# Kernel optimization log

Measured on AMD Instinct MI355X. Metric: run time of the kernel, lower is better.

The kernel has to match this reference:

```python
import jax, jax.numpy as jnp
import numpy as np

N = 50000      # nodes (src == dst, num_layers=1)
F_IN = 256     # feats_dim
HID = 128      # hidden_dim
H = 8          # num_heads
D = HID // H   # per-head dim
E = 800000     # edges per metapath
M = 3          # metapaths
OUT = 8        # out_dim
NEG_SLOPE = 0.2


def setup_inputs() -> dict:
    key = jax.random.key(0)
    ks = jax.random.split(key, 14)
    s = 0.05
    return {
        "features": jax.random.normal(ks[0], (N, F_IN), jnp.float32),
        "W_fc": jax.random.normal(ks[1], (F_IN, HID), jnp.float32) * s,
        "b_fc": jnp.zeros((HID,), jnp.float32),
        "W_src": jax.random.normal(ks[2], (M, HID, HID), jnp.float32) * s,
        "W_dst": jax.random.normal(ks[3], (M, HID, HID), jnp.float32) * s,
        "attn_l": jax.random.normal(ks[4], (M, H, D), jnp.float32) * s,
        "attn_r": jax.random.normal(ks[5], (M, H, D), jnp.float32) * s,
        "W_sem1": jax.random.normal(ks[6], (HID, HID), jnp.float32) * s,
        "b_sem1": jnp.zeros((HID,), jnp.float32),
        "w_sem2": jax.random.normal(ks[7], (HID,), jnp.float32) * s,
        "W_out": jax.random.normal(ks[8], (HID, OUT), jnp.float32) * s,
        "b_out": jnp.zeros((OUT,), jnp.float32),
        "src_idx": jax.random.randint(ks[9], (M, E), 0, N, jnp.int32),
        "dst_idx": jax.random.randint(ks[10], (M, E), 0, N, jnp.int32),
    }


def _gat_conv(h, Wsrc, Wdst, al, ar, src, dst):
    # h: (N, HID); per-metapath GATConv with tuple in_feats (separate src/dst fc)
    fs = (h @ Wsrc).reshape(N, H, D)   # src projected features
    fd = (h @ Wdst).reshape(N, H, D)   # dst projected features
    el = jnp.sum(fs * al, axis=-1)     # (N, H)
    er = jnp.sum(fd * ar, axis=-1)     # (N, H)
    e = jax.nn.leaky_relu(el[src] + er[dst], NEG_SLOPE)  # (E, H)
    # edge softmax segmented by destination node
    mx = jax.ops.segment_max(e, dst, num_segments=N)     # (N, H)
    ex = jnp.exp(e - mx[dst])
    ssum = jax.ops.segment_sum(ex, dst, num_segments=N)  # (N, H)
    alpha = ex / jnp.maximum(ssum[dst], 1e-9)            # (E, H)
    # weighted message aggregation (gather -> scale -> scatter-add)
    out = jax.ops.segment_sum(fs[src] * alpha[:, :, None], dst, num_segments=N)
    return out.reshape(N, HID)


def reference(features, W_fc, b_fc, W_src, W_dst, attn_l, attn_r,
              W_sem1, b_sem1, w_sem2, W_out, b_out, src_idx, dst_idx):
    h_ = features @ W_fc + b_fc                          # (N, HID)
    outs = []
    for m in range(M):  # small fixed loop over metapaths
        hm = _gat_conv(h_, W_src[m], W_dst[m], attn_l[m], attn_r[m],
                       src_idx[m], dst_idx[m])
        outs.append(jax.nn.elu(hm))
    z = jnp.stack(outs, axis=1)                          # (N, M, HID)
    # semantic attention over metapaths
    w = jnp.tanh(z @ W_sem1 + b_sem1) @ w_sem2           # (N, M)
    beta = jax.nn.softmax(w, axis=1)
    fused = jnp.sum(beta[:, :, None] * z, axis=1)        # (N, HID)
    logits = fused @ W_out + b_out                       # (N, OUT)
    return logits
```

## Files before the change

kernel.cpp:

```cpp
#include <hip/hip_runtime.h>
#include <hip/hip_bf16.h>
#include <stdint.h>

#define N_NODES 50000
#define F_IN 256
#define HID 128
#define NH 8
#define DH 16
#define NE 800000
#define NM 3
#define NOUT 8
#define NEG 0.2f
#define NROWS (N_NODES * NM)
#define LDH 136
#define BSH 8
#define NBUCK 196
#define EPB 8192

#define WFCP_N 65536
#define WSP_N  98304
#define UTP_N  6144
#define W1P_N  16384

typedef __attribute__((ext_vector_type(8))) short bfrag;
typedef __attribute__((ext_vector_type(4))) float f32x4;
union FU { uint4 u; bfrag b; };

#define MFMA(a, b, c) __builtin_amdgcn_mfma_f32_16x16x32_bf16(a, b, c, 0, 0, 0)

__device__ __forceinline__ float bf2f(unsigned short u) {
    union { unsigned int ui; float f; } cv;
    cv.ui = ((unsigned int)u) << 16;
    return cv.f;
}
__device__ __forceinline__ unsigned short f2bf(float x) {
    __hip_bfloat16 b = __float2bfloat16(x);
    return reinterpret_cast<const unsigned short&>(b);
}
__device__ __forceinline__ float bflo(unsigned int u) {
    union { unsigned int x; float f; } c; c.x = u << 16; return c.f;
}
__device__ __forceinline__ float bfhi(unsigned int u) {
    union { unsigned int x; float f; } c; c.x = u & 0xffff0000u; return c.f;
}

__global__ __launch_bounds__(256) void k_bhist(const int* __restrict__ dst0,
                                               int* __restrict__ bcnt) {
    __shared__ int cnt[NBUCK];
    int m = blockIdx.y;
    const int* dst = dst0 + (size_t)m * NE;
    int t = threadIdx.x;
    int e0 = blockIdx.x * EPB;
    int e1 = e0 + EPB; if (e1 > NE) e1 = NE;
    for (int i = t; i < NBUCK; i += 256) cnt[i] = 0;
    __syncthreads();
    for (int i = e0 + t; i < e1; i += 256)
        atomicAdd(&cnt[dst[i] >> BSH], 1);
    __syncthreads();
    for (int i = t; i < NBUCK; i += 256)
        if (cnt[i]) atomicAdd(&bcnt[m * NBUCK + i], cnt[i]);
}

__global__ __launch_bounds__(256) void k_bscan(const int* __restrict__ bcnt,
                                               int* __restrict__ bbase,
                                               int* __restrict__ binCur) {
    __shared__ int sc[256];
    int m = blockIdx.x, t = threadIdx.x;
    int v = (t < NBUCK) ? bcnt[m * NBUCK + t] : 0;
    sc[t] = v;
    __syncthreads();
    #pragma unroll
    for (int o = 1; o < 256; o <<= 1) {
        int add = (t >= o) ? sc[t - o] : 0;
        __syncthreads();
        sc[t] += add;
        __syncthreads();
    }
    if (t < NBUCK) {
        int p = sc[t] - v;
        bbase[m * NBUCK + t] = p;
        binCur[m * NBUCK + t] = p;
    }
}

__global__ __launch_bounds__(256) void k_binA2(const int* __restrict__ src0,
                                               const int* __restrict__ dst0,
                                               int* __restrict__ binCur0,
                                               int2* __restrict__ pairs0) {
    __shared__ int cnt[NBUCK];
    __shared__ int base[NBUCK];
    int m = blockIdx.y;
    const int* src = src0 + (size_t)m * NE;
    const int* dst = dst0 + (size_t)m * NE;
    int* binCur = binCur0 + (size_t)m * NBUCK;
    int2* pairs = pairs0 + (size_t)m * NE;
    int t = threadIdx.x;
    int e0 = blockIdx.x * EPB;
    int e1 = e0 + EPB; if (e1 > NE) e1 = NE;
    for (int i = t; i < NBUCK; i += 256) cnt[i] = 0;
    __syncthreads();
    for (int i = e0 + t; i < e1; i += 256)
        atomicAdd(&cnt[dst[i] >> BSH], 1);
    __syncthreads();
    for (int i = t; i < NBUCK; i += 256) {
        int c = cnt[i];
        base[i] = c ? atomicAdd(&binCur[i], c) : 0;
        cnt[i] = 0;
    }
    __syncthreads();
    for (int i = e0 + t; i < e1; i += 256) {
        int d = dst[i], s = src[i];
        int b = d >> BSH;
        int off = atomicAdd(&cnt[b], 1);
        pairs[base[b] + off] = make_int2(s, d);
    }
}

__global__ __launch_bounds__(256) void k_csr(const int2* __restrict__ pairs0,
                                             const int* __restrict__ bcnt,
                                             const int* __restrict__ bbase,
                                             int* __restrict__ offs0,
                                             int* __restrict__ ssrc0) {
    __shared__ int cnt[256];
    __shared__ int cur[256];
    int b = blockIdx.x, m = blockIdx.y, t = threadIdx.x;
    const int2* pairs = pairs0 + (size_t)m * NE;
    int* offs = offs0 + (size_t)m * (N_NODES + 1);
    int* ssrc = ssrc0 + (size_t)m * NE;
    int pbase = bbase[m * NBUCK + b];
    int pend  = pbase + bcnt[m * NBUCK + b];
    cnt[t] = 0;
    __syncthreads();
    for (int i = pbase + t; i < pend; i += 256)
        atomicAdd(&cnt[pairs[i].y & 255], 1);
    __syncthreads();
    int v = cnt[t];
    __syncthreads();
    #pragma unroll
    for (int o = 1; o < 256; o <<= 1) {
        int add = (t >= o) ? cnt[t - o] : 0;
        __syncthreads();
        cnt[t] += add;
        __syncthreads();
    }
    int ex = cnt[t] - v;
    int dst0 = b << BSH;
    int nd = N_NODES - dst0; if (nd > 256) nd = 256;
    if (t < nd) offs[dst0 + t] = pbase + ex;
    if (b == NBUCK - 1 && t == 0) offs[N_NODES] = NE;
    cur[t] = pbase + ex;
    __syncthreads();
    for (int i = pbase + t; i < pend; i += 256) {
        int2 p = pairs[i];
        int pos = atomicAdd(&cur[p.y & 255], 1);
        ssrc[pos] = p.x;
    }
}

__global__ __launch_bounds__(256) void k_pack(const float* __restrict__ Wfc,
                                              const float* __restrict__ Wsrc,
                                              const float* __restrict__ Wdst,
                                              const float* __restrict__ al,
                                              const float* __restrict__ ar,
                                              const float* __restrict__ Wsem1,
                                              unsigned short* __restrict__ wfcph,
                                              unsigned short* __restrict__ wfcpl,
                                              unsigned short* __restrict__ wsph,
                                              unsigned short* __restrict__ wspl,
                                              unsigned short* __restrict__ utph,
                                              unsigned short* __restrict__ utpl,
                                              unsigned short* __restrict__ w1ph,
                                              unsigned short* __restrict__ w1pl) {
    int g = blockIdx.x * 256 + threadIdx.x;
    if (blockIdx.x < 16) {
        int s = g;
        int lane = s & 63, t = s >> 6;
        int ks = t & 7, ct = t >> 3;
        int n = ct * 16 + (lane & 15);
        int kb = ks * 32 + ((lane >> 4) << 3);
        #pragma unroll
        for (int j = 0; j < 8; j++) {
            float v = Wfc[(size_t)(kb + j) * HID + n];
            unsigned short h = f2bf(v);
            wfcph[(size_t)s * 8 + j] = h;
            wfcpl[(size_t)s * 8 + j] = f2bf(v - bf2f(h));
        }
    } else if (blockIdx.x < 40) {
        int s = g - 16 * 256;
        int lane = s & 63, t = s >> 6;
        int ks = t & 3, ct = (t >> 2) & 7, m = t >> 5;
        int n = ct * 16 + (lane & 15);
        int kb = ks * 32 + ((lane >> 4) << 3);
        #pragma unroll
        for (int j = 0; j < 8; j++) {
            float v = Wsrc[((size_t)m * HID + kb + j) * HID + n];
            unsigned short h = f2bf(v);
            wsph[(size_t)s * 8 + j] = h;
            wspl[(size_t)s * 8 + j] = f2bf(v - bf2f(h));
        }
    } else if (blockIdx.x < 43) {
        int s = g - 40 * 256;
        if (s >= UTP_N / 8) return;
        int lane = s & 63, t = s >> 6;
        int ks = t & 3, m = t >> 2;
        int n = lane & 15;
        int kb = ks * 32 + ((lane >> 4) << 3);
        int hh = n & 7;
        const float* W = (n < 8) ? Wsrc : Wdst;
        const float* a = (n < 8) ? al : ar;
        #pragma unroll
        for (int j = 0; j < 8; j++) {
            int k = kb + j;
            const float* wr = W + ((size_t)m * HID + k) * HID + hh * DH;
            const float* av = a + m * HID + hh * DH;
            float v = 0.f;
            #pragma unroll
            for (int d = 0; d < DH; d++) v += wr[d] * av[d];
            unsigned short h = f2bf(v);
            utph[(size_t)s * 8 + j] = h;
            utpl[(size_t)s * 8 + j] = f2bf(v - bf2f(h));
        }
    } else {
        int s = g - 43 * 256;
        int lane = s & 63, t = s >> 6;
        int ks = t & 3, ct = t >> 2;
        int n = ct * 16 + (lane & 15);
        int kb = ks * 32 + ((lane >> 4) << 3);
        #pragma unroll
        for (int j = 0; j < 8; j++) {
            float v = Wsem1[(size_t)(kb + j) * HID + n];
            unsigned short h = f2bf(v);
            w1ph[(size_t)s * 8 + j] = h;
            w1pl[(size_t)s * 8 + j] = f2bf(v - bf2f(h));
        }
    }
}

__global__ __launch_bounds__(256) void k_fcproj(const float* __restrict__ A,
                                                const float* __restrict__ bias,
                                                const unsigned short* __restrict__ wfcph,
                                                const unsigned short* __restrict__ wfcpl,
                                                const unsigned short* __restrict__ wsph,
                                                const unsigned short* __restrict__ wspl,
                                                const unsigned short* __restrict__ utph,
                                                const unsigned short* __restrict__ utpl,
                                                unsigned short* __restrict__ fs0,
                                                float* __restrict__ el0,
                                                float* __restrict__ er0) {
    __shared__ unsigned short hb[64 * LDH];
    int tid = threadIdx.x;
    int w = tid >> 6, l = tid & 63;
    int rw = w & 1;
    int ch = w >> 1;
    int lr = l & 15;
    int lq = l >> 4;
    int r0 = blockIdx.x * 64;
    int gr[2];
    #pragma unroll
    for (int rt = 0; rt < 2; rt++) {
        int rowA = r0 + rw * 32 + rt * 16 + lr;
        gr[rt] = (rowA < N_NODES) ? rowA : (N_NODES - 1);
    }

    f32x4 acc[2][4];
    #pragma unroll
    for (int rt = 0; rt < 2; rt++)
        #pragma unroll
        for (int c = 0; c < 4; c++) acc[rt][c] = (f32x4){0.f, 0.f, 0.f, 0.f};
    const uint4* bh4 = (const uint4*)wfcph;
    const uint4* bl4 = (const uint4*)wfcpl;
    for (int ks = 0; ks < 8; ks++) {
        bfrag ah[2], al_[2];
        #pragma unroll
        for (int rt = 0; rt < 2; rt++) {
            const float* ap = A + (size_t)gr[rt] * F_IN + ks * 32 + lq * 8;
            float4 v0 = ((const float4*)ap)[0];
            float4 v1 = ((const float4*)ap)[1];
            float av[8] = {v0.x, v0.y, v0.z, v0.w, v1.x, v1.y, v1.z, v1.w};
            #pragma unroll
            for (int j = 0; j < 8; j++) {
                unsigned short h = f2bf(av[j]);
                ah[rt][j] = (short)h;
                al_[rt][j] = (short)f2bf(av[j] - bf2f(h));
            }
        }
        #pragma unroll
        for (int c = 0; c < 4; c++) {
            int ct = ch * 4 + c;
            FU bh, bl;
            bh.u = bh4[(ct * 8 + ks) * 64 + l];
            bl.u = bl4[(ct * 8 + ks) * 64 + l];
            #pragma unroll
            for (int rt = 0; rt < 2; rt++) {
                acc[rt][c] = MFMA(ah[rt], bh.b, acc[rt][c]);
                acc[rt][c] = MFMA(ah[rt], bl.b, acc[rt][c]);
                acc[rt][c] = MFMA(al_[rt], bh.b, acc[rt][c]);
            }
        }
    }
    #pragma unroll
    for (int c = 0; c < 4; c++) {
        int col = (ch * 4 + c) * 16 + lr;
        float bb = bias[col];
        #pragma unroll
        for (int rt = 0; rt < 2; rt++)
            #pragma unroll
            for (int rg = 0; rg < 4; rg++) {
                int rloc = rw * 32 + rt * 16 + lq * 4 + rg;
                hb[rloc * LDH + col] = f2bf(acc[rt][c][rg] + bb);
            }
    }
    __syncthreads();
    const uint4* sh4 = (const uint4*)wsph;
    const uint4* sl4 = (const uint4*)wspl;
    const uint4* uh4 = (const uint4*)utph;
    const uint4* ul4 = (const uint4*)utpl;
    for (int m = 0; m < NM; m++) {
        f32x4 acc2[2][4];
        f32x4 eacc[2];
        #pragma unroll
        for (int rt = 0; rt < 2; rt++) {
            eacc[rt] = (f32x4){0.f, 0.f, 0.f, 0.f};
            #pragma unroll
            for (int c = 0; c < 4; c++) acc2[rt][c] = (f32x4){0.f, 0.f, 0.f, 0.f};
        }
        #pragma unroll
        for (int ks = 0; ks < 4; ks++) {
            FU a[2];
            #pragma unroll
            for (int rt = 0; rt < 2; rt++)
                a[rt].u = *(const uint4*)&hb[(rw * 32 + rt * 16 + lr) * LDH + ks * 32 + lq * 8];
            #pragma unroll
            for (int c = 0; c < 4; c++) {
                int ct = ch * 4 + c;
                FU bh, bl;
                bh.u = sh4[(m * 32 + ct * 4 + ks) * 64 + l];
                bl.u = sl4[(m * 32 + ct * 4 + ks) * 64 + l];
                #pragma unroll
                for (int rt = 0; rt < 2; rt++) {
                    acc2[rt][c] = MFMA(a[rt].b, bh.b, acc2[rt][c]);
                    acc2[rt][c] = MFMA(a[rt].b, bl.b, acc2[rt][c]);
                }
            }
            if (ch == 0) {
                FU uh, ul;
                uh.u = uh4[(m * 4 + ks) * 64 + l];
                ul.u = ul4[(m * 4 + ks) * 64 + l];
                #pragma unroll
                for (int rt = 0; rt < 2; rt++) {
                    eacc[rt] = MFMA(a[rt].b, uh.b, eacc[rt]);
                    eacc[rt] = MFMA(a[rt].b, ul.b, eacc[rt]);
                }
            }
        }
        unsigned short* fsm = fs0 + (size_t)m * N_NODES * HID;
        #pragma unroll
        for (int rt = 0; rt < 2; rt++)
            #pragma unroll
            for (int c = 0; c < 4; c++) {
                #pragma unroll
                for (int rg = 0; rg < 4; rg++) {
                    int row = r0 + rw * 32 + rt * 16 + lq * 4 + rg;
                    if (row < N_NODES)
                        fsm[(size_t)row * HID + (ch * 4 + c) * 16 + lr] = f2bf(acc2[rt][c][rg]);
                }
            }
        if (ch == 0) {
            float* elm = el0 + (size_t)m * N_NODES * NH;
            float* erm = er0 + (size_t)m * N_NODES * NH;
            #pragma unroll
            for (int rt = 0; rt < 2; rt++)
                #pragma unroll
                for (int rg = 0; rg < 4; rg++) {
                    int row = r0 + rw * 32 + rt * 16 + lq * 4 + rg;
                    if (row < N_NODES) {
                        if (lr < 8) elm[(size_t)row * NH + lr] = eacc[rt][rg];
                        else        erm[(size_t)row * NH + (lr - 8)] = eacc[rt][rg];
                    }
                }
        }
    }
}

__global__ __launch_bounds__(128) void k_gat(const int* __restrict__ ssrc0,
                                             const int* __restrict__ offs0,
                                             const float* __restrict__ el0,
                                             const float* __restrict__ er0,
                                             const unsigned short* __restrict__ fs0,
                                             float* __restrict__ z) {
    int m = blockIdx.y;
    const int* ssrc = ssrc0 + (size_t)m * NE;
    const int* offs = offs0 + (size_t)m * (N_NODES + 1);
    const float* el = el0 + (size_t)m * N_NODES * NH;
    const float* er = er0 + (size_t)m * N_NODES * NH;
    const unsigned int* fsu = (const unsigned int*)(fs0 + (size_t)m * N_NODES * HID);
    int d = blockIdx.x * 2 + (threadIdx.x >> 6);
    int lane = threadIdx.x & 63;
    int hh = lane >> 3;
    int sub = lane & 7;
    int gbase = lane & 56;
    int s0 = offs[d], s1 = offs[d + 1];
    float erd = er[(unsigned)d * NH + hh];
    float num0 = 0.f, num1 = 0.f, denp = 0.f;
    int base = s0;
    for (; base + 8 <= s1; base += 8) {
        int s = ssrc[base + sub];
        float x = el[(unsigned)s * NH + hh] + erd;
        x = (x >= 0.f) ? x : NEG * x;
        float w = __expf(x);
        denp += w;
        int st[8]; float wt[8];
        #pragma unroll
        for (int t = 0; t < 8; t++) {
            st[t] = __shfl(s, gbase + t, 64);
            wt[t] = __shfl(w, gbase + t, 64);
        }
        unsigned int u[8];
        #pragma unroll
        for (int t = 0; t < 8; t++)
            u[t] = fsu[(unsigned)st[t] * (HID / 2) + lane];
        #pragma unroll
        for (int t = 0; t < 8; t++) {
            num0 += wt[t] * bflo(u[t]);
            num1 += wt[t] * bfhi(u[t]);
        }
    }
    int n = s1 - base;
    if (n > 0) {
        int s = ssrc[base + ((sub < n) ? sub : n - 1)];
        float x = el[(unsigned)s * NH + hh] + erd;
        x = (x >= 0.f) ? x : NEG * x;
        float w = (sub < n) ? __expf(x) : 0.f;
        denp += w;
        #pragma unroll 2
        for (int t = 0; t < n; t++) {
            int st = __shfl(s, gbase + t, 64);
            float wt = __shfl(w, gbase + t, 64);
            unsigned int u = fsu[(unsigned)st * (HID / 2) + lane];
            num0 += wt * bflo(u);
            num1 += wt * bfhi(u);
        }
    }
    denp += __shfl_xor(denp, 1, 64);
    denp += __shfl_xor(denp, 2, 64);
    denp += __shfl_xor(denp, 4, 64);
    float inv = 1.f / fmaxf(denp, 1e-9f);
    float v0 = num0 * inv, v1 = num1 * inv;
    v0 = (v0 > 0.f) ? v0 : (__expf(v0) - 1.f);
    v1 = (v1 > 0.f) ? v1 : (__expf(v1) - 1.f);
    *(float2*)&z[((size_t)d * NM + m) * HID + 2 * lane] = make_float2(v0, v1);
}

__global__ __launch_bounds__(256) void k_semw(const float* __restrict__ A,
                                              const unsigned short* __restrict__ w1ph,
                                              const unsigned short* __restrict__ w1pl,
                                              const float* __restrict__ b1,
                                              const float* __restrict__ ws2,
                                              float* __restrict__ w) {
    int tid = threadIdx.x;
    int wv = tid >> 6, l = tid & 63;
    int lr = l & 15;
    int lq = l >> 4;
    int tbase = blockIdx.x * 64 + wv * 16;
    int rowA = tbase + lr;
    int gr = (rowA < NROWS) ? rowA : (NROWS - 1);
    const uint4* bh4 = (const uint4*)w1ph;
    const uint4* bl4 = (const uint4*)w1pl;
    f32x4 acc[8];
    #pragma unroll
    for (int ct = 0; ct < 8; ct++) acc[ct] = (f32x4){0.f, 0.f, 0.f, 0.f};
    #pragma unroll
    for (int ks = 0; ks < 4; ks++) {
        const float* ap = A + (size_t)gr * HID + ks * 32 + lq * 8;
        float4 v0 = ((const float4*)ap)[0];
        float4 v1 = ((const float4*)ap)[1];
        float av[8] = {v0.x, v0.y, v0.z, v0.w, v1.x, v1.y, v1.z, v1.w};
        bfrag a;
        #pragma unroll
        for (int j = 0; j < 8; j++) a[j] = (short)f2bf(av[j]);
        #pragma unroll
        for (int ct = 0; ct < 8; ct++) {
            FU bh, bl;
            bh.u = bh4[(ct * 4 + ks) * 64 + l];
            bl.u = bl4[(ct * 4 + ks) * 64 + l];
            acc[ct] = MFMA(a, bh.b, acc[ct]);
            acc[ct] = MFMA(a, bl.b, acc[ct]);
        }
    }
    float bb[8], s2[8];
    #pragma unroll
    for (int ct = 0; ct < 8; ct++) {
        bb[ct] = b1[ct * 16 + lr];
        s2[ct] = ws2[ct * 16 + lr];
    }
    #pragma unroll
    for (int rg = 0; rg < 4; rg++) {
        float v = 0.f;
        #pragma unroll
        for (int ct = 0; ct < 8; ct++)
            v += tanhf(acc[ct][rg] + bb[ct]) * s2[ct];
        v += __shfl_xor(v, 1, 64);
        v += __shfl_xor(v, 2, 64);
        v += __shfl_xor(v, 4, 64);
        v += __shfl_xor(v, 8, 64);
        int row = tbase + lq * 4 + rg;
        if (lr == 0 && row < NROWS) w[row] = v;
    }
}

__global__ __launch_bounds__(256) void k_comb(const float* __restrict__ zel,
                                              const float* __restrict__ w,
                                              const float* __restrict__ Wout,
                                              const float* __restrict__ bout,
                                              float* __restrict__ out) {
    __shared__ float fusedL[2][HID];
    int half = threadIdx.x >> 7;
    int j = threadIdx.x & 127;
    int n = blockIdx.x * 2 + half;
    float w0 = w[n * NM + 0];
    float w1 = w[n * NM + 1];
    float w2 = w[n * NM + 2];
    float mx = fmaxf(w0, fmaxf(w1, w2));
    float e0 = __expf(w0 - mx);
    float e1 = __expf(w1 - mx);
    float e2 = __expf(w2 - mx);
    float inv = 1.f / (e0 + e1 + e2);
    size_t base = (size_t)n * NM * HID;
    float f = (e0 * zel[base + j] + e1 * zel[base + HID + j] + e2 * zel[base + 2 * HID + j]) * inv;
    fusedL[half][j] = f;
    __syncthreads();
    int c = j >> 4, t16 = j & 15;
    float p = 0.f;
    #pragma unroll
    for (int i = 0; i < 8; i++) {
        int jj = t16 + i * 16;
        p += fusedL[half][jj] * Wout[jj * NOUT + c];
    }
    #pragma unroll
    for (int o = 8; o > 0; o >>= 1) p += __shfl_down(p, o, 16);
    if (t16 == 0) out[n * NOUT + c] = p + bout[c];
}

extern "C" void kernel_launch(void* const* d_in, const int* in_sizes, int n_in,
                              void* d_out, int out_size, void* d_ws, size_t ws_size,
                              hipStream_t stream) {
    (void)in_sizes; (void)n_in; (void)out_size; (void)ws_size;
    const float* feat  = (const float*)d_in[0];
    const float* Wfc   = (const float*)d_in[1];
    const float* bfc   = (const float*)d_in[2];
    const float* Wsrc  = (const float*)d_in[3];
    const float* Wdst  = (const float*)d_in[4];
    const float* al    = (const float*)d_in[5];
    const float* ar    = (const float*)d_in[6];
    const float* Wsem1 = (const float*)d_in[7];
    const float* bsem1 = (const float*)d_in[8];
    const float* wsem2 = (const float*)d_in[9];
    const float* Wout  = (const float*)d_in[10];
    const float* bout  = (const float*)d_in[11];
    const int* srcI    = (const int*)d_in[12];
    const int* dstI    = (const int*)d_in[13];
    float* out = (float*)d_out;

    float* z    = (float*)d_ws;
    float* el   = z  + (size_t)NROWS * HID;
    float* er   = el + (size_t)NM * N_NODES * NH;
    float* wsc  = er + (size_t)NM * N_NODES * NH;
    unsigned short* wfcph = (unsigned short*)(wsc + (size_t)NROWS);
    unsigned short* wfcpl = wfcph + WFCP_N;
    unsigned short* wsph  = wfcpl + WFCP_N;
    unsigned short* wspl  = wsph + WSP_N;
    unsigned short* utph  = wspl + WSP_N;
    unsigned short* utpl  = utph + UTP_N;
    unsigned short* w1ph  = utpl + UTP_N;
    unsigned short* w1pl  = w1ph + W1P_N;
    unsigned short* fs16  = w1pl + W1P_N;
    int* offs   = (int*)(fs16 + (size_t)NM * N_NODES * HID);
    int* ssrc   = offs   + (size_t)NM * (N_NODES + 1);
    int* bcnt   = ssrc   + (size_t)NM * NE;
    int* bbase  = bcnt   + (size_t)NM * NBUCK;
    int* binCur = bbase  + (size_t)NM * NBUCK;
    int2* pairs = (int2*)fs16;

    hipMemsetAsync(bcnt, 0, (size_t)NM * NBUCK * sizeof(int), stream);
    {
        dim3 gb((NE + EPB - 1) / EPB, NM);
        k_bhist<<<gb, 256, 0, stream>>>(dstI, bcnt);
        k_bscan<<<NM, 256, 0, stream>>>(bcnt, bbase, binCur);
        k_binA2<<<gb, 256, 0, stream>>>(srcI, dstI, binCur, pairs);
        dim3 gcs(NBUCK, NM);
        k_csr<<<gcs, 256, 0, stream>>>(pairs, bcnt, bbase, offs, ssrc);
    }

    k_pack<<<51, 256, 0, stream>>>(Wfc, Wsrc, Wdst, al, ar, Wsem1,
                                   wfcph, wfcpl, wsph, wspl, utph, utpl,
                                   w1ph, w1pl);
    k_fcproj<<<(N_NODES + 63) / 64, 256, 0, stream>>>(feat, bfc,
                                                      wfcph, wfcpl, wsph, wspl,
                                                      utph, utpl, fs16, el, er);
    {
        dim3 gg(N_NODES / 2, NM);
        k_gat<<<gg, 128, 0, stream>>>(ssrc, offs, el, er, fs16, z);
    }

    k_semw<<<(NROWS + 63) / 64, 256, 0, stream>>>(z, w1ph, w1pl, bsem1, wsem2, wsc);
    k_comb<<<N_NODES / 2, 256, 0, stream>>>(z, wsc, Wout, bout, out);
}
```

Before: 523.2 us.

## Fuse semantic scoring with combine, merge bucket scan into pack, pack pairs

Merges the semantic attention score kernel and the combine/output kernel into one kernel. Each 96-row block keeps its scores in shared memory and reuses its z rows, which removes the global score buffer and one launch. The bucket prefix scan moves into the weight-pack kernel as three extra blocks, removing another launch. Binned (src,dst) pairs shrink from int2 to one 32-bit word holding a 16-bit src and 8-bit local dst. That halves the pair traffic but silently truncates src indices above 65535, which only holds because N is 50000.

```diff
diff --git a/kernel.cpp b/kernel.cpp
--- a/kernel.cpp
+++ b/kernel.cpp
@@ -61,39 +61,17 @@
         if (cnt[i]) atomicAdd(&bcnt[m * NBUCK + i], cnt[i]);
 }
 
-__global__ __launch_bounds__(256) void k_bscan(const int* __restrict__ bcnt,
-                                               int* __restrict__ bbase,
-                                               int* __restrict__ binCur) {
-    __shared__ int sc[256];
-    int m = blockIdx.x, t = threadIdx.x;
-    int v = (t < NBUCK) ? bcnt[m * NBUCK + t] : 0;
-    sc[t] = v;
-    __syncthreads();
-    #pragma unroll
-    for (int o = 1; o < 256; o <<= 1) {
-        int add = (t >= o) ? sc[t - o] : 0;
-        __syncthreads();
-        sc[t] += add;
-        __syncthreads();
-    }
-    if (t < NBUCK) {
-        int p = sc[t] - v;
-        bbase[m * NBUCK + t] = p;
-        binCur[m * NBUCK + t] = p;
-    }
-}
-
 __global__ __launch_bounds__(256) void k_binA2(const int* __restrict__ src0,
                                                const int* __restrict__ dst0,
                                                int* __restrict__ binCur0,
-                                               int2* __restrict__ pairs0) {
+                                               unsigned int* __restrict__ pairs0) {
     __shared__ int cnt[NBUCK];
     __shared__ int base[NBUCK];
     int m = blockIdx.y;
     const int* src = src0 + (size_t)m * NE;
     const int* dst = dst0 + (size_t)m * NE;
     int* binCur = binCur0 + (size_t)m * NBUCK;
-    int2* pairs = pairs0 + (size_t)m * NE;
+    unsigned int* pairs = pairs0 + (size_t)m * NE;
     int t = threadIdx.x;
     int e0 = blockIdx.x * EPB;
     int e1 = e0 + EPB; if (e1 > NE) e1 = NE;
@@ -112,11 +90,11 @@
         int d = dst[i], s = src[i];
         int b = d >> BSH;
         int off = atomicAdd(&cnt[b], 1);
-        pairs[base[b] + off] = make_int2(s, d);
-    }
-}
-
-__global__ __launch_bounds__(256) void k_csr(const int2* __restrict__ pairs0,
+        pairs[base[b] + off] = (unsigned int)s | ((unsigned int)(d & 255) << 16);
+    }
+}
+
+__global__ __launch_bounds__(256) void k_csr(const unsigned int* __restrict__ pairs0,
                                              const int* __restrict__ bcnt,
                                              const int* __restrict__ bbase,
                                              int* __restrict__ offs0,
@@ -124,7 +102,7 @@
     __shared__ int cnt[256];
     __shared__ int cur[256];
     int b = blockIdx.x, m = blockIdx.y, t = threadIdx.x;
-    const int2* pairs = pairs0 + (size_t)m * NE;
+    const unsigned int* pairs = pairs0 + (size_t)m * NE;
     int* offs = offs0 + (size_t)m * (N_NODES + 1);
     int* ssrc = ssrc0 + (size_t)m * NE;
     int pbase = bbase[m * NBUCK + b];
@@ -132,7 +110,7 @@
     cnt[t] = 0;
     __syncthreads();
     for (int i = pbase + t; i < pend; i += 256)
-        atomicAdd(&cnt[pairs[i].y & 255], 1);
+        atomicAdd(&cnt[pairs[i] >> 16], 1);
     __syncthreads();
     int v = cnt[t];
     __syncthreads();
@@ -151,9 +129,9 @@
     cur[t] = pbase + ex;
     __syncthreads();
     for (int i = pbase + t; i < pend; i += 256) {
-        int2 p = pairs[i];
-        int pos = atomicAdd(&cur[p.y & 255], 1);
-        ssrc[pos] = p.x;
+        unsigned int p = pairs[i];
+        int pos = atomicAdd(&cur[p >> 16], 1);
+        ssrc[pos] = (int)(p & 0xFFFFu);
     }
 }
 
@@ -163,6 +141,9 @@
                                               const float* __restrict__ al,
                                               const float* __restrict__ ar,
                                               const float* __restrict__ Wsem1,
+                                              const int* __restrict__ bcnt,
+                                              int* __restrict__ bbase,
+                                              int* __restrict__ binCur,
                                               unsigned short* __restrict__ wfcph,
                                               unsigned short* __restrict__ wfcpl,
                                               unsigned short* __restrict__ wsph,
@@ -171,6 +152,7 @@
                                               unsigned short* __restrict__ utpl,
                                               unsigned short* __restrict__ w1ph,
                                               unsigned short* __restrict__ w1pl) {
+    __shared__ int sc[256];
     int g = blockIdx.x * 256 + threadIdx.x;
     if (blockIdx.x < 16) {
         int s = g;
@@ -220,7 +202,7 @@
             utph[(size_t)s * 8 + j] = h;
             utpl[(size_t)s * 8 + j] = f2bf(v - bf2f(h));
         }
-    } else {
+    } else if (blockIdx.x < 51) {
         int s = g - 43 * 256;
         int lane = s & 63, t = s >> 6;
         int ks = t & 3, ct = t >> 2;
@@ -232,6 +214,23 @@
             unsigned short h = f2bf(v);
             w1ph[(size_t)s * 8 + j] = h;
             w1pl[(size_t)s * 8 + j] = f2bf(v - bf2f(h));
+        }
+    } else {
+        int m = blockIdx.x - 51, t = threadIdx.x;
+        int v = (t < NBUCK) ? bcnt[m * NBUCK + t] : 0;
+        sc[t] = v;
+        __syncthreads();
+        #pragma unroll
+        for (int o = 1; o < 256; o <<= 1) {
+            int add = (t >= o) ? sc[t - o] : 0;
+            __syncthreads();
+            sc[t] += add;
+            __syncthreads();
+        }
+        if (t < NBUCK) {
+            int p = sc[t] - v;
+            bbase[m * NBUCK + t] = p;
+            binCur[m * NBUCK + t] = p;
         }
     }
 }
@@ -451,17 +450,22 @@
     *(float2*)&z[((size_t)d * NM + m) * HID + 2 * lane] = make_float2(v0, v1);
 }
 
-__global__ __launch_bounds__(256) void k_semw(const float* __restrict__ A,
-                                              const unsigned short* __restrict__ w1ph,
-                                              const unsigned short* __restrict__ w1pl,
-                                              const float* __restrict__ b1,
-                                              const float* __restrict__ ws2,
-                                              float* __restrict__ w) {
+__global__ __launch_bounds__(384) void k_semcomb(const float* __restrict__ A,
+                                                 const unsigned short* __restrict__ w1ph,
+                                                 const unsigned short* __restrict__ w1pl,
+                                                 const float* __restrict__ b1,
+                                                 const float* __restrict__ ws2,
+                                                 const float* __restrict__ Wout,
+                                                 const float* __restrict__ bout,
+                                                 float* __restrict__ out) {
+    __shared__ float wsL[96];
+    __shared__ float fusedL[3][HID];
     int tid = threadIdx.x;
     int wv = tid >> 6, l = tid & 63;
     int lr = l & 15;
     int lq = l >> 4;
-    int tbase = blockIdx.x * 64 + wv * 16;
+    int r0 = blockIdx.x * 96;
+    int tbase = r0 + wv * 16;
     int rowA = tbase + lr;
     int gr = (rowA < NROWS) ? rowA : (NROWS - 1);
     const uint4* bh4 = (const uint4*)w1ph;
@@ -504,41 +508,46 @@
         v += __shfl_xor(v, 4, 64);
         v += __shfl_xor(v, 8, 64);
         int row = tbase + lq * 4 + rg;
-        if (lr == 0 && row < NROWS) w[row] = v;
-    }
-}
-
-__global__ __launch_bounds__(256) void k_comb(const float* __restrict__ zel,
-                                              const float* __restrict__ w,
-                                              const float* __restrict__ Wout,
-                                              const float* __restrict__ bout,
-                                              float* __restrict__ out) {
-    __shared__ float fusedL[2][HID];
-    int half = threadIdx.x >> 7;
-    int j = threadIdx.x & 127;
-    int n = blockIdx.x * 2 + half;
-    float w0 = w[n * NM + 0];
-    float w1 = w[n * NM + 1];
-    float w2 = w[n * NM + 2];
-    float mx = fmaxf(w0, fmaxf(w1, w2));
-    float e0 = __expf(w0 - mx);
-    float e1 = __expf(w1 - mx);
-    float e2 = __expf(w2 - mx);
-    float inv = 1.f / (e0 + e1 + e2);
-    size_t base = (size_t)n * NM * HID;
-    float f = (e0 * zel[base + j] + e1 * zel[base + HID + j] + e2 * zel[base + 2 * HID + j]) * inv;
-    fusedL[half][j] = f;
-    __syncthreads();
-    int c = j >> 4, t16 = j & 15;
-    float p = 0.f;
-    #pragma unroll
-    for (int i = 0; i < 8; i++) {
-        int jj = t16 + i * 16;
-        p += fusedL[half][jj] * Wout[jj * NOUT + c];
-    }
-    #pragma unroll
-    for (int o = 8; o > 0; o >>= 1) p += __shfl_down(p, o, 16);
-    if (t16 == 0) out[n * NOUT + c] = p + bout[c];
+        if (lr == 0 && row < NROWS) wsL[row - r0] = v;
+    }
+    __syncthreads();
+    int n0 = r0 / 3;
+    int snb = tid >> 7;
+    int j = tid & 127;
+    #pragma unroll 1
+    for (int p = 0; p < 11; p++) {
+        int nn = p * 3 + snb;
+        int n = n0 + nn;
+        bool ok = (nn < 32) && (n < N_NODES);
+        if (ok) {
+            float w0 = wsL[nn * 3 + 0];
+            float w1 = wsL[nn * 3 + 1];
+            float w2 = wsL[nn * 3 + 2];
+            float mx = fmaxf(w0, fmaxf(w1, w2));
+            float e0 = __expf(w0 - mx);
+            float e1 = __expf(w1 - mx);
+            float e2 = __expf(w2 - mx);
+            float inv = 1.f / (e0 + e1 + e2);
+            size_t base = (size_t)n * NM * HID;
+            float f = (e0 * A[base + j] + e1 * A[base + HID + j]
+                       + e2 * A[base + 2 * HID + j]) * inv;
+            fusedL[snb][j] = f;
+        }
+        __syncthreads();
+        if (ok) {
+            int c = j >> 4, t16 = j & 15;
+            float pa = 0.f;
+            #pragma unroll
+            for (int i = 0; i < 8; i++) {
+                int jj = t16 + i * 16;
+                pa += fusedL[snb][jj] * Wout[jj * NOUT + c];
+            }
+            #pragma unroll
+            for (int o = 8; o > 0; o >>= 1) pa += __shfl_down(pa, o, 16);
+            if (t16 == 0) out[n * NOUT + c] = pa + bout[c];
+        }
+        __syncthreads();
+    }
 }
 
 extern "C" void kernel_launch(void* const* d_in, const int* in_sizes, int n_in,
@@ -564,8 +573,7 @@
     float* z    = (float*)d_ws;
     float* el   = z  + (size_t)NROWS * HID;
     float* er   = el + (size_t)NM * N_NODES * NH;
-    float* wsc  = er + (size_t)NM * N_NODES * NH;
-    unsigned short* wfcph = (unsigned short*)(wsc + (size_t)NROWS);
+    unsigned short* wfcph = (unsigned short*)(er + (size_t)NM * N_NODES * NH);
     unsigned short* wfcpl = wfcph + WFCP_N;
     unsigned short* wsph  = wfcpl + WFCP_N;
     unsigned short* wspl  = wsph + WSP_N;
@@ -579,21 +587,21 @@
     int* bcnt   = ssrc   + (size_t)NM * NE;
     int* bbase  = bcnt   + (size_t)NM * NBUCK;
     int* binCur = bbase  + (size_t)NM * NBUCK;
-    int2* pairs = (int2*)fs16;
+    unsigned int* pairs = (unsigned int*)fs16;
 
     hipMemsetAsync(bcnt, 0, (size_t)NM * NBUCK * sizeof(int), stream);
     {
         dim3 gb((NE + EPB - 1) / EPB, NM);
         k_bhist<<<gb, 256, 0, stream>>>(dstI, bcnt);
-        k_bscan<<<NM, 256, 0, stream>>>(bcnt, bbase, binCur);
+        k_pack<<<54, 256, 0, stream>>>(Wfc, Wsrc, Wdst, al, ar, Wsem1,
+                                       bcnt, bbase, binCur,
+                                       wfcph, wfcpl, wsph, wspl, utph, utpl,
+                                       w1ph, w1pl);
         k_binA2<<<gb, 256, 0, stream>>>(srcI, dstI, binCur, pairs);
         dim3 gcs(NBUCK, NM);
         k_csr<<<gcs, 256, 0, stream>>>(pairs, bcnt, bbase, offs, ssrc);
     }
 
-    k_pack<<<51, 256, 0, stream>>>(Wfc, Wsrc, Wdst, al, ar, Wsem1,
-                                   wfcph, wfcpl, wsph, wspl, utph, utpl,
-                                   w1ph, w1pl);
     k_fcproj<<<(N_NODES + 63) / 64, 256, 0, stream>>>(feat, bfc,
                                                       wfcph, wfcpl, wsph, wspl,
                                                       utph, utpl, fs16, el, er);
@@ -602,6 +610,6 @@
         k_gat<<<gg, 128, 0, stream>>>(ssrc, offs, el, er, fs16, z);
     }
 
-    k_semw<<<(NROWS + 63) / 64, 256, 0, stream>>>(z, w1ph, w1pl, bsem1, wsem2, wsc);
-    k_comb<<<N_NODES / 2, 256, 0, stream>>>(z, wsc, Wout, bout, out);
-}
+    k_semcomb<<<(NROWS + 95) / 96, 384, 0, stream>>>(z, w1ph, w1pl, bsem1, wsem2,
+                                                     Wout, bout, out);
+}
```

New measurement: 515.9 us. Within noise of the previous version (-1.4%).
